# Performance work log

Measured on AMD Instinct MI355X. Metric: run time of the kernel, lower is better.

## Reference

```python
import jax, jax.numpy as jnp
import numpy as np

N_VERTICES = 2000
N_SENSORY = 784
N_EDGES = 500_000
BATCH = 32
T_STEPS = 5
LR_VALUES = 0.1


def setup_inputs() -> dict:
    key = jax.random.key(0)
    k1, k2, k3 = jax.random.split(key, 3)
    values = jax.random.normal(k1, (BATCH, N_VERTICES), dtype=jnp.float32)
    # weight_init 'normal 0.0' -> std = max(0.01, 0) = 0.01 in the torch module
    weights = jax.random.normal(k2, (N_EDGES,), dtype=jnp.float32) * 0.01
    edge_index = jax.random.randint(k3, (2, N_EDGES), 0, N_VERTICES, dtype=jnp.int32)
    # sensory nodes (first 784) are clamped; only internal nodes update
    update_mask = jnp.arange(N_VERTICES) >= N_SENSORY  # bool [N]
    return {
        "values": values,
        "weights": weights,
        "edge_index": edge_index,
        "update_mask": update_mask,
        "T": T_STEPS,
    }


def reference(values, weights, edge_index, update_mask, T):
    """Iterative predictive-coding message passing.

    Each step:
      pred_i  = sum_{e: dst(e)=i} w_e * f(values[src(e)])   (gather-mul-scatter)
      err     = values - pred
      back_j  = sum_{e: src(e)=j} w_e * err[dst(e)]          (reverse scatter)
      dv      = err - f'(values) * back                      (dE/dx)
      values  = values - lr * dv   (sensory nodes clamped)
    """
    src, dst = edge_index[0], edge_index[1]
    n = values.shape[1]
    mask = update_mask[None, :]

    def step(v, _):
        fx = jnp.tanh(v)                                   # [B, N]
        msg = weights[None, :] * fx[:, src]                # [B, E]
        pred = jax.ops.segment_sum(msg.T, dst, num_segments=n).T  # [B, N]
        err = v - pred                                     # [B, N]
        w_err = weights[None, :] * err[:, dst]             # [B, E]
        back = jax.ops.segment_sum(w_err.T, src, num_segments=n).T  # [B, N]
        fprime = 1.0 - fx * fx                             # tanh'
        dv = err - fprime * back
        v_new = jnp.where(mask, v - LR_VALUES * dv, v)
        return v_new, None

    v_final, _ = jax.lax.scan(step, values, None, length=T)
    return v_final
```

## Files before the change

### kernel.cpp

```cpp
#include <hip/hip_runtime.h>
#include <hip/hip_bf16.h>


#define N_V     2000
#define N_SENS  784
#define N_INT   (N_V - N_SENS)
#define N_E     500000
#define T_STEPS 5
#define LR_VAL  0.1f
#define NVB     (N_V * 32)
#define NVH     (N_V * 16)
#define KP      2016
#define NCH     63
#define NT1     125
#define NT2     76
#define FRAG_N  (2 * NCH * 64 * 8)
#define NBLK    250
#define EPB     2000
#define NBLK_P  250
#define BAR_STRIDE 32
#define BAR_N   ((NBLK_P + 1) * BAR_STRIDE)

typedef float  f32x4 __attribute__((ext_vector_type(4)));
typedef short  s16x8 __attribute__((ext_vector_type(8)));
typedef unsigned long long u64;

__device__ __forceinline__ float bits_to_f32(unsigned u) {
    union { unsigned u; float f; } c; c.u = u; return c.f;
}
__device__ __forceinline__ unsigned f32_to_bits(float f) {
    union { float f; unsigned u; } c; c.f = f; return c.u;
}
__device__ __forceinline__ unsigned short f32_to_bf16(float f) {
    unsigned u = f32_to_bits(f);
    return (unsigned short)((u + 0x7FFFu + ((u >> 16) & 1u)) >> 16);
}
__device__ __forceinline__ float bf16_to_f32(unsigned short s) {
    return bits_to_f32((unsigned)s << 16);
}

__device__ __forceinline__ u64 ald64(const void* p) {
    return __hip_atomic_load((const u64*)p, __ATOMIC_RELAXED,
                             __HIP_MEMORY_SCOPE_AGENT);
}
__device__ __forceinline__ void ast64(void* p, u64 v) {
    __hip_atomic_store((u64*)p, v, __ATOMIC_RELAXED, __HIP_MEMORY_SCOPE_AGENT);
}
__device__ __forceinline__ unsigned short ald16(const unsigned short* p) {
    return __hip_atomic_load(p, __ATOMIC_RELAXED, __HIP_MEMORY_SCOPE_AGENT);
}
__device__ __forceinline__ void ast16(unsigned short* p, unsigned short v) {
    __hip_atomic_store(p, v, __ATOMIC_RELAXED, __HIP_MEMORY_SCOPE_AGENT);
}
__device__ __forceinline__ int cohld(const int* p) {
    int v;
    asm volatile("global_load_dword %0, %1, off sc0 sc1\n\ts_waitcnt vmcnt(0)"
                 : "=v"(v) : "v"(p) : "memory");
    return v;
}
__device__ __forceinline__ void cohst(int* p, int v) {
    asm volatile("global_store_dword %0, %1, off sc0 sc1"
                 :: "v"(p), "v"(v) : "memory");
}

__device__ __forceinline__ int aposKB(int k, int b) {
    int c = k >> 5, q = (k >> 3) & 3, j = k & 7;
    int h = b >> 4, m = b & 15;
    return (((h * NCH + c) * 64) + q * 16 + m) * 8 + j;
}


__global__ __launch_bounds__(256) void k_cnt(const int* __restrict__ dst,
                                             int* __restrict__ cnt_g,
                                             unsigned short* __restrict__ fxA,
                                             unsigned short* __restrict__ errA,
                                             const float* __restrict__ vin,
                                             float* __restrict__ v,
                                             float* __restrict__ out,
                                             unsigned short* __restrict__ WAdT,
                                             int* __restrict__ bar) {
    __shared__ int cnt[NT1];
    int b = blockIdx.x;
    int t = b * 256 + threadIdx.x;
    {
        if (t < 16 * 32) {
            int k = 2000 + (t >> 5), bb = t & 31;
            fxA[aposKB(k, bb)] = 0;
            errA[aposKB(k, bb)] = 0;
        }
        if (t < N_INT * 2) {
            uint4 z = {0u, 0u, 0u, 0u};
            *(uint4*)(WAdT + (size_t)(t >> 1) * KP + 2000 + (t & 1) * 8) = z;
        }
        if (t < BAR_N) bar[t] = 0;
    }
    if (t < NVB) {
        float x = vin[t];
        int bb = t / N_V;
        int i = t - bb * N_V;
        v[(i << 5) + bb] = x;
        fxA[aposKB(i, bb)] = f32_to_bf16(tanhf(x));
        if (i < N_SENS) out[t] = x;
    }
    for (int i = threadIdx.x; i < NT1; i += 256) cnt[i] = 0;
    __syncthreads();
    int base = b * EPB;
    for (int e = base + threadIdx.x; e < base + EPB; e += 256)
        atomicAdd(&cnt[dst[e] >> 4], 1);
    __syncthreads();
    for (int tt = threadIdx.x; tt < NT1; tt += 256)
        cnt_g[tt * 256 + b] = cnt[tt];
}

__global__ __launch_bounds__(256) void k_scan_a(const int* __restrict__ cnt_g,
                                                int* __restrict__ base_g,
                                                int* __restrict__ totals) {
    __shared__ int sh[256];
    int t = blockIdx.x, tid = threadIdx.x;
    int v = (tid < NBLK) ? cnt_g[t * 256 + tid] : 0;
    sh[tid] = v;
    __syncthreads();
    for (int off = 1; off < 256; off <<= 1) {
        int x = (tid >= off) ? sh[tid - off] : 0;
        __syncthreads();
        sh[tid] += x;
        __syncthreads();
    }
    if (tid < NBLK) base_g[t * 256 + tid] = sh[tid] - v;
    if (tid == 255) totals[t] = sh[255];
}

__global__ __launch_bounds__(256) void k_place(
        const int* __restrict__ src, const int* __restrict__ dst,
        const float* __restrict__ w, const int* __restrict__ base_g,
        const int* __restrict__ totals, unsigned* __restrict__ pk_g) {
    __shared__ int cur[NT1];
    __shared__ int ts[NT1];
    int b = blockIdx.x;
    if (threadIdx.x == 0) {
        int a = 0;
        for (int t = 0; t < NT1; ++t) { ts[t] = a; a += totals[t]; }
    }
    __syncthreads();
    for (int t = threadIdx.x; t < NT1; t += 256)
        cur[t] = ts[t] + base_g[t * 256 + b];
    __syncthreads();
    int base = b * EPB;
    for (int e = base + threadIdx.x; e < base + EPB; e += 256) {
        int d = dst[e];
        unsigned pk = ((unsigned)f32_to_bf16(w[e]) << 16)
                    | ((unsigned)(d & 15) << 11) | (unsigned)src[e];
        int p = atomicAdd(&cur[d >> 4], 1);
        pk_g[p] = pk;
    }
}

__global__ __launch_bounds__(256) void k_build(
        const unsigned* __restrict__ pk_g, const int* __restrict__ totals,
        uint4* __restrict__ WAbf4, unsigned short* __restrict__ WAdT) {
    __shared__ float acc[16][KP];
    __shared__ int ts[NT1 + 1];
    int tile = blockIdx.x;
    for (int i = threadIdx.x; i < 16 * KP / 4; i += 256)
        ((float4*)&acc[0][0])[i] = make_float4(0.f, 0.f, 0.f, 0.f);
    if (threadIdx.x == 0) {
        int a = 0;
        for (int t = 0; t < NT1; ++t) { ts[t] = a; a += totals[t]; }
        ts[NT1] = a;
    }
    __syncthreads();
    int beg = ts[tile], end = ts[tile + 1];
    for (int e = beg + threadIdx.x; e < end; e += 256) {
        unsigned pk = pk_g[e];
        int row = (int)((pk >> 11) & 15u);
        atomicAdd(&acc[row][pk & 0x7FFu], bf16_to_f32((unsigned short)(pk >> 16)));
    }
    __syncthreads();
    for (int i = threadIdx.x; i < 16 * 252; i += 256) {
        int m = i / 252, g = i - m * 252;
        int c = g >> 2, q = g & 3;
        int col = g * 8;
        unsigned short r[8];
        #pragma unroll
        for (int j = 0; j < 8; ++j) r[j] = f32_to_bf16(acc[m][col + j]);
        WAbf4[((tile * NCH + c) * 64) + q * 16 + m] = *(const uint4*)r;
    }
    for (int i = threadIdx.x; i < N_INT; i += 256) {
        int j = N_SENS + i;
        unsigned short r[16];
        #pragma unroll
        for (int m = 0; m < 16; ++m) r[m] = f32_to_bf16(acc[m][j]);
        uint4* p = (uint4*)(WAdT + (size_t)i * KP + tile * 16);
        p[0] = *(const uint4*)r;
        p[1] = *(const uint4*)(r + 8);
    }
}

__device__ __forceinline__ void gbar(int* arr, int epoch, int bx, int tid) {
    asm volatile("s_waitcnt vmcnt(0) lgkmcnt(0)" ::: "memory");
    __syncthreads();
    if (bx == 0) {
        if (tid == 0) cohst(&arr[0], epoch);
        if (tid < NBLK_P) {
            while (cohld(&arr[tid * BAR_STRIDE]) < epoch)
                __builtin_amdgcn_s_sleep(2);
        }
        __syncthreads();
        if (tid == 0) cohst(&arr[NBLK_P * BAR_STRIDE], epoch);
    } else {
        if (tid == 0) {
            cohst(&arr[bx * BAR_STRIDE], epoch);
            while (cohld(&arr[NBLK_P * BAR_STRIDE]) < epoch)
                __builtin_amdgcn_s_sleep(2);
        }
        __syncthreads();
    }
}

__global__ __launch_bounds__(512, 1) void k_loop(
        const uint4* __restrict__ WAbf4, const unsigned short* __restrict__ WAdT,
        unsigned short* fxA, unsigned short* errA,
        float* v_cur, float* __restrict__ out, int* arr) {
    __shared__ uint4 WldsA[NCH * 64];
    __shared__ uint4 WldsB[NCH * 64];
    __shared__ float red[2600];
    const int bx = blockIdx.x, tid = threadIdx.x;
    const int tile = bx >> 1, h = bx & 1;
    {
        const uint4* Wg = WAbf4 + (size_t)tile * (NCH * 64);
        for (int i = tid; i < NCH * 64; i += 512) WldsA[i] = Wg[i];
        if (bx < 2 * NT2) {
            for (int i = tid; i < NCH * 64; i += 512) {
                int c = i >> 6, ll = i & 63;
                int row = tile * 16 + (ll & 15);
                int k0 = c * 32 + (ll >> 4) * 8;
                WldsB[i] = *(const uint4*)(WAdT + (size_t)row * KP + k0);
            }
        }
    }
    const int w = tid >> 6, l = tid & 63;
    const int cbeg = w * 8;
    float* my = &red[w * 325 + l * 5];
    int epoch = 0;
    __syncthreads();

    for (int t = 0; t < T_STEPS; ++t) {
        {
            const u64* ap = (const u64*)fxA
                          + ((size_t)h * (NCH * 64) + cbeg * 64 + l) * 2;
            u64 f0[8], f1[8];
            #pragma unroll
            for (int cc = 0; cc < 8; ++cc)
                if (cbeg + cc < NCH) {
                    f0[cc] = ald64(ap + cc * 128);
                    f1[cc] = ald64(ap + cc * 128 + 1);
                }
            __builtin_amdgcn_sched_barrier(0);
            f32x4 acc = {0.f, 0.f, 0.f, 0.f};
            #pragma unroll
            for (int cc = 0; cc < 8; ++cc)
                if (cbeg + cc < NCH) {
                    u64 d[2] = {f0[cc], f1[cc]};
                    uint4 bfrag = WldsA[(cbeg + cc) * 64 + l];
                    acc = __builtin_amdgcn_mfma_f32_16x16x32_bf16(
                              *(s16x8*)d, *(s16x8*)&bfrag, acc, 0, 0, 0);
                }
            #pragma unroll
            for (int r = 0; r < 4; ++r) my[r] = acc[r];
            __syncthreads();
            if (w == 0) {
                float s[4];
                #pragma unroll
                for (int r = 0; r < 4; ++r) {
                    float sum = 0.f;
                    #pragma unroll
                    for (int ww = 0; ww < 8; ++ww)
                        sum += red[ww * 325 + l * 5 + r];
                    s[r] = sum;
                }
                int i = tile * 16 + (l & 15);
                int q = l >> 4;
                int c2 = i >> 5, q2 = (i >> 3) & 3, j2 = i & 7;
                const float* vp = v_cur + (i << 5) + h * 16 + q * 4;
                union { u64 u[2]; float f[4]; } vu;
                vu.u[0] = ald64(vp);
                vu.u[1] = ald64(vp + 2);
                int base = ((h * NCH + c2) * 64 + q2 * 16) * 8 + j2;
                #pragma unroll
                for (int r = 0; r < 4; ++r)
                    ast16(&errA[base + (q * 4 + r) * 8],
                          f32_to_bf16(vu.f[r] - s[r]));
            }
        }
        ++epoch; gbar(arr, epoch, bx, tid);

        if (bx < 2 * NT2) {
            const u64* ap = (const u64*)errA
                          + ((size_t)h * (NCH * 64) + cbeg * 64 + l) * 2;
            u64 f0[8], f1[8];
            #pragma unroll
            for (int cc = 0; cc < 8; ++cc)
                if (cbeg + cc < NCH) {
                    f0[cc] = ald64(ap + cc * 128);
                    f1[cc] = ald64(ap + cc * 128 + 1);
                }
            __builtin_amdgcn_sched_barrier(0);
            f32x4 acc = {0.f, 0.f, 0.f, 0.f};
            #pragma unroll
            for (int cc = 0; cc < 8; ++cc)
                if (cbeg + cc < NCH) {
                    u64 d[2] = {f0[cc], f1[cc]};
                    uint4 bfrag = WldsB[(cbeg + cc) * 64 + l];
                    acc = __builtin_amdgcn_mfma_f32_16x16x32_bf16(
                              *(s16x8*)d, *(s16x8*)&bfrag, acc, 0, 0, 0);
                }
            #pragma unroll
            for (int r = 0; r < 4; ++r) my[r] = acc[r];
            __syncthreads();
            if (w == 0) {
                float s[4];
                #pragma unroll
                for (int r = 0; r < 4; ++r) {
                    float sum = 0.f;
                    #pragma unroll
                    for (int ww = 0; ww < 8; ++ww)
                        sum += red[ww * 325 + l * 5 + r];
                    s[r] = sum;
                }
                int j = N_SENS + tile * 16 + (l & 15);
                int q = l >> 4;
                int c2 = j >> 5, q2 = (j >> 3) & 3, j2 = j & 7;
                float* vp = v_cur + (j << 5) + h * 16 + q * 4;
                union { u64 u[2]; float f[4]; } vu;
                vu.u[0] = ald64(vp);
                vu.u[1] = ald64(vp + 2);
                int base = ((h * NCH + c2) * 64 + q2 * 16) * 8 + j2;
                #pragma unroll
                for (int r = 0; r < 4; ++r) {
                    float e0 = bf16_to_f32(ald16(&errA[base + (q * 4 + r) * 8]));
                    float fxv = tanhf(vu.f[r]);
                    float vn = vu.f[r] - LR_VAL * (e0 - (1.f - fxv * fxv) * s[r]);
                    vu.f[r] = vn;
                    ast16(&fxA[base + (q * 4 + r) * 8], f32_to_bf16(tanhf(vn)));
                }
                ast64(vp, vu.u[0]);
                ast64(vp + 2, vu.u[1]);
                if (t == T_STEPS - 1) {
                    #pragma unroll
                    for (int r = 0; r < 4; ++r) {
                        int b = h * 16 + q * 4 + r;
                        out[b * N_V + j] = vu.f[r];
                    }
                }
            }
        }
        if (t < T_STEPS - 1) { ++epoch; gbar(arr, epoch, bx, tid); }
    }
}


__global__ void k_zero_i32(int* a, int n) {
    int t = blockIdx.x * blockDim.x + threadIdx.x;
    if (t < n) a[t] = 0;
}

__global__ void k_hist(const int* __restrict__ src, const int* __restrict__ dst,
                       int* cnt_dst, int* cnt_src) {
    int e = blockIdx.x * blockDim.x + threadIdx.x;
    if (e < N_E) {
        atomicAdd(&cnt_dst[dst[e]], 1);
        atomicAdd(&cnt_src[src[e]], 1);
    }
}

__global__ __launch_bounds__(1024) void k_scan(int* cnt_a, int* rp_a,
                                               int* cnt_b, int* rp_b) {
    __shared__ int sh[1024];
    int t = threadIdx.x;
    for (int pass = 0; pass < 2; ++pass) {
        int* cnt = pass ? cnt_b : cnt_a;
        int* rp  = pass ? rp_b  : rp_a;
        int i0 = 2 * t, i1 = 2 * t + 1;
        int c0 = (i0 < N_V) ? cnt[i0] : 0;
        int c1 = (i1 < N_V) ? cnt[i1] : 0;
        __syncthreads();
        sh[t] = c0 + c1;
        __syncthreads();
        for (int off = 1; off < 1024; off <<= 1) {
            int v = (t >= off) ? sh[t - off] : 0;
            __syncthreads();
            sh[t] += v;
            __syncthreads();
        }
        int incl = sh[t];
        int e0 = incl - (c0 + c1);
        int e1 = e0 + c0;
        if (i0 <= N_V) rp[i0] = e0;
        if (i1 <= N_V) rp[i1] = e1;
        if (i0 < N_V) cnt[i0] = e0;
        if (i1 < N_V) cnt[i1] = e1;
    }
}

__global__ void k_scatter(const int* __restrict__ src, const int* __restrict__ dst,
                          const float* __restrict__ w,
                          int* cur_dst, int* cur_src,
                          unsigned* __restrict__ pk_dst, unsigned* __restrict__ pk_src) {
    int e = blockIdx.x * blockDim.x + threadIdx.x;
    if (e < N_E) {
        int s = src[e], d = dst[e];
        unsigned wbits = (unsigned)f32_to_bf16(w[e]);
        int p = atomicAdd(&cur_dst[d], 1);
        pk_dst[p] = (wbits << 16) | (unsigned)s;
        int q = atomicAdd(&cur_src[s], 1);
        pk_src[q] = (wbits << 16) | (unsigned)d;
    }
}

__global__ void k_cast_in(const float* __restrict__ vin, float* __restrict__ v) {
    int t = blockIdx.x * blockDim.x + threadIdx.x;
    if (t < NVB) {
        int i = t >> 5, b = t & 31;
        v[t] = vin[b * N_V + i];
    }
}

__global__ void k_fx_csr(const float* __restrict__ v, unsigned short* __restrict__ fx) {
    int t = blockIdx.x * blockDim.x + threadIdx.x;
    if (t < NVB) {
        int i = t >> 5, b = t & 31;
        int h = b >> 4, b16 = b & 15;
        fx[h * NVH + i * 16 + b16] = f32_to_bf16(tanhf(v[t]));
    }
}

__global__ __launch_bounds__(256) void k_pred_err(
        const float* __restrict__ v, const unsigned short* __restrict__ fx,
        const int* __restrict__ rp, const unsigned* __restrict__ pk,
        unsigned short* __restrict__ err) {
    __shared__ unsigned short tab[NVH];
    int h  = blockIdx.x / 250;
    int vg = blockIdx.x % 250;
    {
        const uint4* g = (const uint4*)(fx + h * NVH);
        uint4* l = (uint4*)tab;
        for (int i = threadIdx.x; i < NVH / 8; i += 256) l[i] = g[i];
    }
    __syncthreads();
    int wave = threadIdx.x >> 6;
    int lane = threadIdx.x & 63;
    int b16 = lane & 15, epar = lane >> 4;
    for (int k = 0; k < 2; ++k) {
        int vid = vg * 8 + wave * 2 + k;
        int beg = rp[vid], end = rp[vid + 1];
        float sum = 0.f;
        for (int e = beg + epar; e < end; e += 4) {
            unsigned p = pk[e];
            float w = bits_to_f32(p & 0xFFFF0000u);
            int nb = (int)(p & 0xFFFFu);
            sum += w * bf16_to_f32(tab[nb * 16 + b16]);
        }
        sum += __shfl_xor(sum, 16, 64);
        sum += __shfl_xor(sum, 32, 64);
        if (epar == 0) {
            float vo = v[(vid << 5) + h * 16 + b16];
            err[h * NVH + vid * 16 + b16] = f32_to_bf16(vo - sum);
        }
    }
}

__global__ __launch_bounds__(256) void k_back_upd(
        const unsigned short* __restrict__ fx, const unsigned short* __restrict__ err,
        const int* __restrict__ rp, const unsigned* __restrict__ pk,
        float* __restrict__ v) {
    __shared__ unsigned short tab[NVH];
    int h  = blockIdx.x / 152;
    int vg = blockIdx.x % 152;
    {
        const uint4* g = (const uint4*)(err + h * NVH);
        uint4* l = (uint4*)tab;
        for (int i = threadIdx.x; i < NVH / 8; i += 256) l[i] = g[i];
    }
    __syncthreads();
    int wave = threadIdx.x >> 6;
    int lane = threadIdx.x & 63;
    int b16 = lane & 15, epar = lane >> 4;
    for (int k = 0; k < 2; ++k) {
        int vid = N_SENS + vg * 8 + wave * 2 + k;
        if (vid >= N_V) continue;
        int beg = rp[vid], end = rp[vid + 1];
        float sum = 0.f;
        for (int e = beg + epar; e < end; e += 4) {
            unsigned p = pk[e];
            float w = bits_to_f32(p & 0xFFFF0000u);
            int nb = (int)(p & 0xFFFFu);
            sum += w * bf16_to_f32(tab[nb * 16 + b16]);
        }
        sum += __shfl_xor(sum, 16, 64);
        sum += __shfl_xor(sum, 32, 64);
        if (epar == 0) {
            float e0  = bf16_to_f32(tab[vid * 16 + b16]);
            float fxv = bf16_to_f32(fx[h * NVH + vid * 16 + b16]);
            float dv = e0 - (1.f - fxv * fxv) * sum;
            v[(vid << 5) + h * 16 + b16] -= LR_VAL * dv;
        }
    }
}

__global__ void k_out_fb(const float* __restrict__ v, float* __restrict__ out) {
    int t = blockIdx.x * blockDim.x + threadIdx.x;
    if (t < NVB) {
        int b = t / N_V;
        int i = t - b * N_V;
        out[t] = v[(i << 5) + b];
    }
}


extern "C" void kernel_launch(void* const* d_in, const int* in_sizes, int n_in,
                              void* d_out, int out_size, void* d_ws, size_t ws_size,
                              hipStream_t stream) {
    const float* vals = (const float*)d_in[0];
    const float* wts  = (const float*)d_in[1];
    const int* ei = (const int*)d_in[2];
    const int* src = ei;
    const int* dst = ei + N_E;
    float* out = (float*)d_out;

    const int EB = (N_E + 255) / 256;

    const size_t WABF_T = (size_t)NT1 * NCH * 64;
    const size_t WADT_N = (size_t)N_INT * KP;
    const size_t need = (size_t)N_E * 4 + 2 * NT1 * 256 * 4 + 512
                      + WADT_N * 2 + WABF_T * 16
                      + 2 * (size_t)FRAG_N * 2 + NVB * 4
                      + (size_t)BAR_N * 4 + 256;

    if (ws_size >= need) {
        unsigned* pk_g = (unsigned*)d_ws;
        int* cnt_g  = (int*)(pk_g + N_E);
        int* base_g = cnt_g + NT1 * 256;
        int* totals = base_g + NT1 * 256;
        unsigned short* WAdT = (unsigned short*)(totals + 128);
        uint4* WAbf4 = (uint4*)(WAdT + WADT_N);
        unsigned short* fxA  = (unsigned short*)(WAbf4 + WABF_T);
        unsigned short* errA = fxA + FRAG_N;
        float* v_cur = (float*)(errA + FRAG_N);
        int* bar_arr = (int*)(v_cur + NVB);

        k_cnt<<<NBLK, 256, 0, stream>>>(dst, cnt_g, fxA, errA, vals, v_cur,
                                        out, WAdT, bar_arr);
        k_scan_a<<<NT1, 256, 0, stream>>>(cnt_g, base_g, totals);
        k_place<<<NBLK, 256, 0, stream>>>(src, dst, wts, base_g, totals, pk_g);
        k_build<<<NT1, 256, 0, stream>>>(pk_g, totals, WAbf4, WAdT);
        k_loop<<<NBLK_P, 512, 0, stream>>>(WAbf4, WAdT, fxA, errA, v_cur, out,
                                           bar_arr);
    } else {
        float* v_cur = (float*)d_ws;
        unsigned short* fx_g  = (unsigned short*)(v_cur + NVB);
        unsigned short* err_g = fx_g + NVB;
        int* rp_dst  = (int*)(err_g + NVB);
        int* rp_src  = rp_dst + 2048;
        int* cur_dst = rp_src + 2048;
        int* cur_src = cur_dst + 2048;
        unsigned* pk_dst = (unsigned*)(cur_src + 2048);
        unsigned* pk_src = pk_dst + N_E;

        k_zero_i32<<<16, 256, 0, stream>>>(cur_dst, 4096);
        k_hist<<<EB, 256, 0, stream>>>(src, dst, cur_dst, cur_src);
        k_scan<<<1, 1024, 0, stream>>>(cur_dst, rp_dst, cur_src, rp_src);
        k_scatter<<<EB, 256, 0, stream>>>(src, dst, wts, cur_dst, cur_src,
                                          pk_dst, pk_src);
        k_cast_in<<<250, 256, 0, stream>>>(vals, v_cur);
        for (int t = 0; t < T_STEPS; ++t) {
            k_fx_csr<<<250, 256, 0, stream>>>(v_cur, fx_g);
            k_pred_err<<<500, 256, 0, stream>>>(v_cur, fx_g, rp_dst, pk_dst, err_g);
            k_back_upd<<<304, 256, 0, stream>>>(fx_g, err_g, rp_src, pk_src, v_cur);
        }
        k_out_fb<<<250, 256, 0, stream>>>(v_cur, out);
    }
}
```

Measured before the change: 149.5 us.

## Precompute clamped sensory contribution to predictions once before the time loop

Sensory node values never change, so their tanh contribution to the forward prediction is constant across steps. A prologue computes the partial MFMA sum over the first 24.5 K-chunks (sensory columns) once and stores it in registers. Each step's forward pass then covers only the remaining internal chunks, with 5 chunks per wave instead of 8. Separately, the weight-building kernel moves to 512 threads per block. The cost is an extra prologue pass and per-wave chunk masking at the boundary chunk.

```diff
diff --git a/kernel.cpp b/kernel.cpp
--- a/kernel.cpp
+++ b/kernel.cpp
@@ -20,6 +20,7 @@
 #define NBLK_P  250
 #define BAR_STRIDE 32
 #define BAR_N   ((NBLK_P + 1) * BAR_STRIDE)
+#define C_SENS  24
 
 typedef float  f32x4 __attribute__((ext_vector_type(4)));
 typedef short  s16x8 __attribute__((ext_vector_type(8)));
@@ -155,13 +156,13 @@
     }
 }
 
-__global__ __launch_bounds__(256) void k_build(
+__global__ __launch_bounds__(512) void k_build(
         const unsigned* __restrict__ pk_g, const int* __restrict__ totals,
         uint4* __restrict__ WAbf4, unsigned short* __restrict__ WAdT) {
     __shared__ float acc[16][KP];
     __shared__ int ts[NT1 + 1];
     int tile = blockIdx.x;
-    for (int i = threadIdx.x; i < 16 * KP / 4; i += 256)
+    for (int i = threadIdx.x; i < 16 * KP / 4; i += 512)
         ((float4*)&acc[0][0])[i] = make_float4(0.f, 0.f, 0.f, 0.f);
     if (threadIdx.x == 0) {
         int a = 0;
@@ -170,13 +171,13 @@
     }
     __syncthreads();
     int beg = ts[tile], end = ts[tile + 1];
-    for (int e = beg + threadIdx.x; e < end; e += 256) {
+    for (int e = beg + threadIdx.x; e < end; e += 512) {
         unsigned pk = pk_g[e];
         int row = (int)((pk >> 11) & 15u);
         atomicAdd(&acc[row][pk & 0x7FFu], bf16_to_f32((unsigned short)(pk >> 16)));
     }
     __syncthreads();
-    for (int i = threadIdx.x; i < 16 * 252; i += 256) {
+    for (int i = threadIdx.x; i < 16 * 252; i += 512) {
         int m = i / 252, g = i - m * 252;
         int c = g >> 2, q = g & 3;
         int col = g * 8;
@@ -185,7 +186,7 @@
         for (int j = 0; j < 8; ++j) r[j] = f32_to_bf16(acc[m][col + j]);
         WAbf4[((tile * NCH + c) * 64) + q * 16 + m] = *(const uint4*)r;
     }
-    for (int i = threadIdx.x; i < N_INT; i += 256) {
+    for (int i = threadIdx.x; i < N_INT; i += 512) {
         int j = N_SENS + i;
         unsigned short r[16];
         #pragma unroll
@@ -239,29 +240,70 @@
         }
     }
     const int w = tid >> 6, l = tid & 63;
-    const int cbeg = w * 8;
+    const int grp = l >> 4;
     float* my = &red[w * 325 + l * 5];
     int epoch = 0;
-    __syncthreads();
+    float pc[4] = {0.f, 0.f, 0.f, 0.f};
+    __syncthreads();
+
+    {
+        const int cb0 = w * 4;
+        const u64* ap = (const u64*)fxA
+                      + ((size_t)h * (NCH * 64) + cb0 * 64 + l) * 2;
+        u64 f0[4], f1[4];
+        #pragma unroll
+        for (int cc = 0; cc < 4; ++cc)
+            if (cb0 + cc <= C_SENS) {
+                f0[cc] = ald64(ap + cc * 128);
+                f1[cc] = ald64(ap + cc * 128 + 1);
+                if (cb0 + cc == C_SENS && grp >= 2) { f0[cc] = 0; f1[cc] = 0; }
+            }
+        __builtin_amdgcn_sched_barrier(0);
+        f32x4 acc = {0.f, 0.f, 0.f, 0.f};
+        #pragma unroll
+        for (int cc = 0; cc < 4; ++cc)
+            if (cb0 + cc <= C_SENS) {
+                u64 d[2] = {f0[cc], f1[cc]};
+                uint4 bfrag = WldsA[(cb0 + cc) * 64 + l];
+                acc = __builtin_amdgcn_mfma_f32_16x16x32_bf16(
+                          *(s16x8*)d, *(s16x8*)&bfrag, acc, 0, 0, 0);
+            }
+        #pragma unroll
+        for (int r = 0; r < 4; ++r) my[r] = acc[r];
+        __syncthreads();
+        if (w == 0) {
+            #pragma unroll
+            for (int r = 0; r < 4; ++r) {
+                float sum = 0.f;
+                #pragma unroll
+                for (int ww = 0; ww < 8; ++ww)
+                    sum += red[ww * 325 + l * 5 + r];
+                pc[r] = sum;
+            }
+        }
+        __syncthreads();
+    }
 
     for (int t = 0; t < T_STEPS; ++t) {
         {
+            const int cb = C_SENS + w * 5;
             const u64* ap = (const u64*)fxA
-                          + ((size_t)h * (NCH * 64) + cbeg * 64 + l) * 2;
-            u64 f0[8], f1[8];
+                          + ((size_t)h * (NCH * 64) + cb * 64 + l) * 2;
+            u64 f0[5], f1[5];
             #pragma unroll
-            for (int cc = 0; cc < 8; ++cc)
-                if (cbeg + cc < NCH) {
+            for (int cc = 0; cc < 5; ++cc)
+                if (cb + cc < NCH) {
                     f0[cc] = ald64(ap + cc * 128);
                     f1[cc] = ald64(ap + cc * 128 + 1);
+                    if (cb + cc == C_SENS && grp < 2) { f0[cc] = 0; f1[cc] = 0; }
                 }
             __builtin_amdgcn_sched_barrier(0);
             f32x4 acc = {0.f, 0.f, 0.f, 0.f};
             #pragma unroll
-            for (int cc = 0; cc < 8; ++cc)
-                if (cbeg + cc < NCH) {
+            for (int cc = 0; cc < 5; ++cc)
+                if (cb + cc < NCH) {
                     u64 d[2] = {f0[cc], f1[cc]};
-                    uint4 bfrag = WldsA[(cbeg + cc) * 64 + l];
+                    uint4 bfrag = WldsA[(cb + cc) * 64 + l];
                     acc = __builtin_amdgcn_mfma_f32_16x16x32_bf16(
                               *(s16x8*)d, *(s16x8*)&bfrag, acc, 0, 0, 0);
                 }
@@ -272,7 +314,7 @@
                 float s[4];
                 #pragma unroll
                 for (int r = 0; r < 4; ++r) {
-                    float sum = 0.f;
+                    float sum = pc[r];
                     #pragma unroll
                     for (int ww = 0; ww < 8; ++ww)
                         sum += red[ww * 325 + l * 5 + r];
@@ -295,12 +337,13 @@
         ++epoch; gbar(arr, epoch, bx, tid);
 
         if (bx < 2 * NT2) {
+            const int cb = w * 8;
             const u64* ap = (const u64*)errA
-                          + ((size_t)h * (NCH * 64) + cbeg * 64 + l) * 2;
+                          + ((size_t)h * (NCH * 64) + cb * 64 + l) * 2;
             u64 f0[8], f1[8];
             #pragma unroll
             for (int cc = 0; cc < 8; ++cc)
-                if (cbeg + cc < NCH) {
+                if (cb + cc < NCH) {
                     f0[cc] = ald64(ap + cc * 128);
                     f1[cc] = ald64(ap + cc * 128 + 1);
                 }
@@ -308,9 +351,9 @@
             f32x4 acc = {0.f, 0.f, 0.f, 0.f};
             #pragma unroll
             for (int cc = 0; cc < 8; ++cc)
-                if (cbeg + cc < NCH) {
+                if (cb + cc < NCH) {
                     u64 d[2] = {f0[cc], f1[cc]};
-                    uint4 bfrag = WldsB[(cbeg + cc) * 64 + l];
+                    uint4 bfrag = WldsB[(cb + cc) * 64 + l];
                     acc = __builtin_amdgcn_mfma_f32_16x16x32_bf16(
                               *(s16x8*)d, *(s16x8*)&bfrag, acc, 0, 0, 0);
                 }
@@ -552,7 +595,7 @@
                                         out, WAdT, bar_arr);
         k_scan_a<<<NT1, 256, 0, stream>>>(cnt_g, base_g, totals);
         k_place<<<NBLK, 256, 0, stream>>>(src, dst, wts, base_g, totals, pk_g);
-        k_build<<<NT1, 256, 0, stream>>>(pk_g, totals, WAbf4, WAdT);
+        k_build<<<NT1, 512, 0, stream>>>(pk_g, totals, WAbf4, WAdT);
         k_loop<<<NBLK_P, 512, 0, stream>>>(WAbf4, WAdT, fxA, errA, v_cur, out,
                                            bar_arr);
     } else {
```

After: 146.9 us. About the same (-1.8%).
